# Performance work log

Hardware: AMD Instinct MI355X
Metric: run time of the kernel (lower is better)

The kernel has to match this reference:

```python
import jax, jax.numpy as jnp
import numpy as np

B, N, C = 4, 2048, 384
H = 6
D = C // H
HID = int(C * 4.0)
EPS = 1e-5


def setup_inputs() -> dict:
    key = jax.random.key(0)
    ks = jax.random.split(key, 12)
    s = lambda fan_in: 1.0 / np.sqrt(fan_in)
    return {
        "x": jax.random.normal(ks[0], (B, N, C), dtype=jnp.float32),
        "ln1_g": jnp.ones((C,), jnp.float32),
        "ln1_b": jnp.zeros((C,), jnp.float32),
        "w_qkv": jax.random.uniform(ks[1], (C, 3 * C), jnp.float32, -s(C), s(C)),
        "w_proj": jax.random.uniform(ks[2], (C, C), jnp.float32, -s(C), s(C)),
        "b_proj": jax.random.uniform(ks[3], (C,), jnp.float32, -s(C), s(C)),
        "ln2_g": jnp.ones((C,), jnp.float32),
        "ln2_b": jnp.zeros((C,), jnp.float32),
        "w_fc1": jax.random.uniform(ks[4], (C, HID), jnp.float32, -s(C), s(C)),
        "b_fc1": jax.random.uniform(ks[5], (HID,), jnp.float32, -s(C), s(C)),
        "w_fc2": jax.random.uniform(ks[6], (HID, C), jnp.float32, -s(HID), s(HID)),
        "b_fc2": jax.random.uniform(ks[7], (C,), jnp.float32, -s(HID), s(HID)),
    }


def _layernorm(x, g, b):
    mu = jnp.mean(x, axis=-1, keepdims=True)
    var = jnp.mean(jnp.square(x - mu), axis=-1, keepdims=True)
    return (x - mu) * jax.lax.rsqrt(var + EPS) * g + b


def reference(x, ln1_g, ln1_b, w_qkv, w_proj, b_proj, ln2_g, ln2_b, w_fc1, b_fc1, w_fc2, b_fc2):
    # --- attention branch (pre-norm) ---
    h = _layernorm(x, ln1_g, ln1_b)                       # [B,N,C]
    qkv = (h @ w_qkv).reshape(B, N, 3, H, D)
    q = jnp.transpose(qkv[:, :, 0], (0, 2, 1, 3))          # [B,H,N,D]
    k = jnp.transpose(qkv[:, :, 1], (0, 2, 1, 3))
    v = jnp.transpose(qkv[:, :, 2], (0, 2, 1, 3))
    scale = D ** -0.5
    attn = jnp.einsum("bhnd,bhmd->bhnm", q, k) * scale     # [B,H,N,N]
    attn = jax.nn.softmax(attn, axis=-1)
    o = jnp.einsum("bhnm,bhmd->bhnd", attn, v)             # [B,H,N,D]
    o = jnp.transpose(o, (0, 2, 1, 3)).reshape(B, N, C)
    x = x + (o @ w_proj + b_proj)
    # --- MLP branch (pre-norm) ---
    h2 = _layernorm(x, ln2_g, ln2_b)
    m = jax.nn.gelu(h2 @ w_fc1 + b_fc1, approximate=False)  # torch nn.GELU = exact erf
    x = x + (m @ w_fc2 + b_fc2)
    return x
```

## Files before the change

kernel.cpp:

```cpp
#include <hip/hip_runtime.h>

typedef __bf16 bf16x8 __attribute__((ext_vector_type(8)));
typedef float f32x4 __attribute__((ext_vector_type(4)));
typedef float f32x16 __attribute__((ext_vector_type(16)));
typedef unsigned short u16;
typedef unsigned int u32;
typedef unsigned long long u64;

#define BB 4
#define NNCTX 2048
#define CCH 384
#define NHEAD 6
#define DHEAD 64
#define HIDDIM 1536

__device__ __forceinline__ u16 f2bf(float f){
  u32 u = __builtin_bit_cast(u32, f);
  u = u + 0x7fffu + ((u >> 16) & 1u);
  return (u16)(u >> 16);
}
__device__ __forceinline__ float bf2f(u16 h){
  u32 u = ((u32)h) << 16;
  return __builtin_bit_cast(float, u);
}

union U8 { uint4 u; u16 s[8]; bf16x8 v; };
union F8 { u32 w[4]; bf16x8 v; };

__global__ __launch_bounds__(256) void cast_tr(const float* __restrict__ w0, const float* __restrict__ w1,
    const float* __restrict__ w2, const float* __restrict__ w3,
    u16* __restrict__ o0, u16* __restrict__ o1, u16* __restrict__ o2, u16* __restrict__ o3){
  __shared__ float S[64][65];
  int idx = blockIdx.x;
  const float* src; u16* dst; int K, N, kt, nt;
  if (idx < 108){ src = w0; dst = o0; K = 384; N = 1152; kt = idx / 18; nt = idx % 18; }
  else if (idx < 144){ idx -= 108; src = w1; dst = o1; K = 384; N = 384; kt = idx / 6; nt = idx % 6; }
  else if (idx < 288){ idx -= 144; src = w2; dst = o2; K = 384; N = 1536; kt = idx / 24; nt = idx % 24; }
  else { idx -= 288; src = w3; dst = o3; K = 1536; N = 384; kt = idx / 6; nt = idx % 6; }
  int t = threadIdx.x;
  int r4 = t >> 6, c = t & 63;
  int k0 = kt * 64, n0 = nt * 64;
  #pragma unroll
  for (int i = 0; i < 16; i++){
    int row = i * 4 + r4;
    S[row][c] = src[(size_t)(k0 + row) * N + n0 + c];
  }
  __syncthreads();
  #pragma unroll
  for (int i = 0; i < 16; i++){
    int row = i * 4 + r4;
    dst[(size_t)(n0 + row) * K + k0 + c] = f2bf(S[c][row]);
  }
}

__global__ __launch_bounds__(128) void ln_kernel(const float* __restrict__ x, const float* __restrict__ g,
                                                 const float* __restrict__ bb, u16* __restrict__ out){
  int row = blockIdx.x, t = threadIdx.x;
  const float* xr = x + (size_t)row * CCH;
  float v0 = xr[t], v1 = xr[t + 128], v2 = xr[t + 256];
  float s = v0 + v1 + v2;
  float q = v0 * v0 + v1 * v1 + v2 * v2;
  #pragma unroll
  for (int o = 32; o; o >>= 1){ s += __shfl_down(s, o); q += __shfl_down(q, o); }
  __shared__ float sh[4];
  if ((t & 63) == 0){ int w = t >> 6; sh[w * 2] = s; sh[w * 2 + 1] = q; }
  __syncthreads();
  float sum = sh[0] + sh[2], ssq = sh[1] + sh[3];
  float mu = sum * (1.0f / 384.0f);
  float rstd = rsqrtf(ssq * (1.0f / 384.0f) - mu * mu + 1e-5f);
  size_t base = (size_t)row * CCH;
  out[base + t]       = f2bf((v0 - mu) * rstd * g[t]       + bb[t]);
  out[base + t + 128] = f2bf((v1 - mu) * rstd * g[t + 128] + bb[t + 128]);
  out[base + t + 256] = f2bf((v2 - mu) * rstd * g[t + 256] + bb[t + 256]);
}

template<int EPI, int DBUF>
__global__ __launch_bounds__(256) void gemm_bf16(const u16* __restrict__ A, const u16* __restrict__ Bt,
    int K, int Nn, u16* __restrict__ outb, const float* __restrict__ bias,
    const float* __restrict__ resid, float* __restrict__ outf)
{
  __shared__ u16 As[DBUF + 1][64][68];
  __shared__ u16 Bs[DBUF + 1][64][68];
  int t = threadIdx.x;
  int bm = blockIdx.y * 64, bn = blockIdx.x * 64;
  int l = t & 63, w = t >> 6;
  int wm = (w >> 1) * 32, wn = (w & 1) * 32;
  f32x4 acc[2][2] = {};
  int ar0 = t >> 3, ac0 = (t & 7) * 8;
  uint4 la0, la1, lb0, lb1;
  auto LOADG = [&](int k0){
    la0 = *(const uint4*)&A[(size_t)(bm + ar0) * K + k0 + ac0];
    la1 = *(const uint4*)&A[(size_t)(bm + ar0 + 32) * K + k0 + ac0];
    lb0 = *(const uint4*)&Bt[(size_t)(bn + ar0) * K + k0 + ac0];
    lb1 = *(const uint4*)&Bt[(size_t)(bn + ar0 + 32) * K + k0 + ac0];
  };
  auto WRITEL = [&](int bf){
    *(uint4*)&As[bf][ar0][ac0]      = la0;
    *(uint4*)&As[bf][ar0 + 32][ac0] = la1;
    *(uint4*)&Bs[bf][ar0][ac0]      = lb0;
    *(uint4*)&Bs[bf][ar0 + 32][ac0] = lb1;
  };
  auto COMPUTE = [&](int bf){
    #pragma unroll
    for (int ks = 0; ks < 2; ks++){
      int kb = ks * 32 + (l >> 4) * 8;
      bf16x8 a0  = *(const bf16x8*)&As[bf][wm + (l & 15)][kb];
      bf16x8 a1  = *(const bf16x8*)&As[bf][wm + 16 + (l & 15)][kb];
      bf16x8 bb0 = *(const bf16x8*)&Bs[bf][wn + (l & 15)][kb];
      bf16x8 bb1 = *(const bf16x8*)&Bs[bf][wn + 16 + (l & 15)][kb];
      acc[0][0] = __builtin_amdgcn_mfma_f32_16x16x32_bf16(a0, bb0, acc[0][0], 0, 0, 0);
      acc[0][1] = __builtin_amdgcn_mfma_f32_16x16x32_bf16(a0, bb1, acc[0][1], 0, 0, 0);
      acc[1][0] = __builtin_amdgcn_mfma_f32_16x16x32_bf16(a1, bb0, acc[1][0], 0, 0, 0);
      acc[1][1] = __builtin_amdgcn_mfma_f32_16x16x32_bf16(a1, bb1, acc[1][1], 0, 0, 0);
    }
  };
  if constexpr (DBUF){
    int nk = K >> 6;
    LOADG(0);
    WRITEL(0);
    __syncthreads();
    for (int ki = 0; ki < nk; ki++){
      int cur = ki & 1;
      if (ki + 1 < nk) LOADG((ki + 1) << 6);
      COMPUTE(cur);
      if (ki + 1 < nk) WRITEL(cur ^ 1);
      __syncthreads();
    }
  } else {
    for (int k0 = 0; k0 < K; k0 += 64){
      __syncthreads();
      LOADG(k0);
      WRITEL(0);
      __syncthreads();
      COMPUTE(0);
    }
  }
  #pragma unroll
  for (int mi = 0; mi < 2; mi++)
  #pragma unroll
  for (int ni = 0; ni < 2; ni++)
  #pragma unroll
  for (int r = 0; r < 4; r++){
    int row = bm + wm + mi * 16 + ((l >> 4) << 2) + r;
    int col = bn + wn + ni * 16 + (l & 15);
    size_t idx = (size_t)row * Nn + col;
    float v = acc[mi][ni][r];
    if (EPI == 0){
      outb[idx] = f2bf(v);
    } else if (EPI == 1){
      outf[idx] = resid[idx] + v + bias[col];
    } else {
      v += bias[col];
      v = 0.5f * v * (1.0f + erff(v * 0.70710678118f));
      outb[idx] = f2bf(v);
    }
  }
}

#define PVSTEP(C2, O0, O1, O2, O3)                                               \
  {                                                                              \
    bf16x8 pf = *(const bf16x8*)&Ps[w][l & 31][(C2) * 16 + hi8];                 \
    u64 ta, tb, tc, td;                                                          \
    asm volatile("ds_read_b64_tr_b16 %0, %4 offset:" #O0 "\n\t"                  \
                 "ds_read_b64_tr_b16 %1, %4 offset:" #O1 "\n\t"                  \
                 "ds_read_b64_tr_b16 %2, %4 offset:" #O2 "\n\t"                  \
                 "ds_read_b64_tr_b16 %3, %4 offset:" #O3 "\n\t"                  \
                 "s_waitcnt lgkmcnt(0)"                                          \
                 : "=&v"(ta), "=&v"(tb), "=&v"(tc), "=&v"(td)                    \
                 : "v"(vtr));                                                    \
    __builtin_amdgcn_sched_barrier(0);                                           \
    F8 f0, f1;                                                                   \
    f0.w[0] = (u32)ta; f0.w[1] = (u32)(ta >> 32);                                \
    f0.w[2] = (u32)tb; f0.w[3] = (u32)(tb >> 32);                                \
    f1.w[0] = (u32)tc; f1.w[1] = (u32)(tc >> 32);                                \
    f1.w[2] = (u32)td; f1.w[3] = (u32)(td >> 32);                                \
    l_acc = __builtin_amdgcn_mfma_f32_32x32x16_bf16(pf, onesf, l_acc, 0, 0, 0);  \
    o_0 = __builtin_amdgcn_mfma_f32_32x32x16_bf16(pf, f0.v, o_0, 0, 0, 0);       \
    o_1 = __builtin_amdgcn_mfma_f32_32x32x16_bf16(pf, f1.v, o_1, 0, 0, 0);       \
  }

__global__ __launch_bounds__(256, 3) void attn_mfma(const u16* __restrict__ qkv,
    u16* __restrict__ o0buf, u16* __restrict__ o1buf, float2* __restrict__ mlbuf){
  __shared__ u16 Ks[64][68];
  __shared__ __attribute__((aligned(128))) u16 Vs[4096];
  __shared__ u16 Ps[4][32][72];
  int t = threadIdx.x;
  int w = t >> 6, l = t & 63;
  int c31 = l & 31, hi = l >> 5, hi8 = hi * 8;
  int id = blockIdx.x;
  int xcd = id & 7, slot = id >> 3;
  int qb = slot & 15;
  int group = (slot >> 4) * 8 + xcd;
  int bh = group % (BB * NHEAD);
  int sp = group / (BB * NHEAD);
  int b = bh / NHEAD, h = bh % NHEAD;
  int q0 = qb * 128;

  const float QS = 0.1803368801111716f;
  bf16x8 qf[4];
  {
    const u16* qp = qkv + (size_t)(b * NNCTX + q0 + w * 32 + c31) * 1152 + h * 64 + hi8;
    #pragma unroll
    for (int c = 0; c < 4; c++){
      U8 r; r.u = *(const uint4*)(qp + c * 16);
      #pragma unroll
      for (int j = 0; j < 8; j++) r.s[j] = f2bf(bf2f(r.s[j]) * QS);
      qf[c] = r.v;
    }
  }
  bf16x8 onesf;
  {
    U8 r;
    #pragma unroll
    for (int j = 0; j < 8; j++) r.s[j] = 0x3F80;
    onesf = r.v;
  }
  f32x16 o_0 = {}, o_1 = {};
  f32x16 l_acc = {};
  float m_r[16];
  #pragma unroll
  for (int r = 0; r < 16; r++) m_r[r] = -3.4e38f;

  const size_t kvrow = (size_t)(b * NNCTX) * 1152 + h * 64;
  int kkey = t >> 2, kdp = (t & 3) * 16;
  int vkey = t & 63, vdblk = (t >> 6) * 16;
  int vj = ((vkey & 31) << 1) | (vkey >> 5);
  int voff = (vj >> 2) * 256 + (vdblk >> 4) * 64 + (vj & 3) * 16;
  int lg = l >> 4, lr = l & 15;
  u32 vtr = (u32)(uintptr_t)(&Vs[0]) + (u32)((lg >> 1) * 1024 + (lg & 1) * 128 + lr * 8);

  uint4 kra, krb, vra, vrb;
  auto LOADT = [&](int kt){
    const u16* kp = qkv + kvrow + (size_t)(kt * 64 + kkey) * 1152 + 384 + kdp;
    kra = *(const uint4*)kp;
    krb = *(const uint4*)(kp + 8);
    const u16* vp = qkv + kvrow + (size_t)(kt * 64 + vkey) * 1152 + 768 + vdblk;
    vra = *(const uint4*)vp;
    vrb = *(const uint4*)(vp + 8);
  };
  auto WRITET = [&](){
    *(uint4*)&Ks[kkey][kdp]     = kra;
    *(uint4*)&Ks[kkey][kdp + 8] = krb;
    *(uint4*)&Vs[voff]     = vra;
    *(uint4*)&Vs[voff + 8] = vrb;
  };

  int ktbeg = sp * 16, ktend = ktbeg + 16;
  LOADT(ktbeg);
  WRITET();
  __syncthreads();

  for (int kt = ktbeg; kt < ktend; kt++){
    if (kt + 1 < ktend) LOADT(kt + 1);

    f32x16 s0 = {}, s1 = {};
    #pragma unroll
    for (int c = 0; c < 4; c++){
      bf16x8 kf0 = *(const bf16x8*)&Ks[c31][c * 16 + hi8];
      bf16x8 kf1 = *(const bf16x8*)&Ks[32 + c31][c * 16 + hi8];
      s0 = __builtin_amdgcn_mfma_f32_32x32x16_bf16(qf[c], kf0, s0, 0, 0, 0);
      s1 = __builtin_amdgcn_mfma_f32_32x32x16_bf16(qf[c], kf1, s1, 0, 0, 0);
    }
    bool ok = true;
    float rml[16];
    #pragma unroll
    for (int r = 0; r < 16; r++){
      rml[r] = fmaxf(s0[r], s1[r]);
      ok = ok && (rml[r] <= m_r[r] + 8.f);
    }
    if (!__all(ok)){
      #pragma unroll
      for (int r = 0; r < 16; r++){
        float mt = rml[r];
        mt = fmaxf(mt, __shfl_xor(mt, 1));
        mt = fmaxf(mt, __shfl_xor(mt, 2));
        mt = fmaxf(mt, __shfl_xor(mt, 4));
        mt = fmaxf(mt, __shfl_xor(mt, 8));
        mt = fmaxf(mt, __shfl_xor(mt, 16));
        float mn = fmaxf(m_r[r], mt);
        float a = __builtin_exp2f(m_r[r] - mn);
        m_r[r] = mn;
        l_acc[r] *= a;
        o_0[r] *= a;
        o_1[r] *= a;
      }
    }
    #pragma unroll
    for (int r = 0; r < 16; r++){
      float p0 = __builtin_exp2f(s0[r] - m_r[r]);
      float p1 = __builtin_exp2f(s1[r] - m_r[r]);
      int crow = (r & 3) + 8 * (r >> 2) + 4 * hi;
      *(u32*)&Ps[w][crow][c31 * 2] = (u32)f2bf(p0) | ((u32)f2bf(p1) << 16);
    }
    PVSTEP(0, 0, 512, 256, 768)
    PVSTEP(1, 2048, 2560, 2304, 2816)
    PVSTEP(2, 4096, 4608, 4352, 4864)
    PVSTEP(3, 6144, 6656, 6400, 6912)

    __syncthreads();
    if (kt + 1 < ktend) WRITET();
    __syncthreads();
  }
  u16* obuf = sp ? o1buf : o0buf;
  #pragma unroll
  for (int r = 0; r < 16; r++){
    int n = q0 + w * 32 + (r & 3) + 8 * (r >> 2) + 4 * hi;
    size_t row = (size_t)(b * NNCTX + n);
    u16* op = obuf + row * CCH + h * 64;
    op[c31]      = f2bf(o_0[r]);
    op[32 + c31] = f2bf(o_1[r]);
    if (c31 == 0)
      mlbuf[((size_t)(sp * BB * NHEAD + bh)) * NNCTX + n] = make_float2(m_r[r], l_acc[r]);
  }
}

__global__ __launch_bounds__(128) void attn_combine(const u16* __restrict__ o0, const u16* __restrict__ o1,
    const float2* __restrict__ ml, u16* __restrict__ obuf){
  __shared__ float sc0[NHEAD], sc1[NHEAD];
  int row = blockIdx.x;
  int b = row >> 11, n = row & 2047;
  int t = threadIdx.x;
  if (t < NHEAD){
    float2 a = ml[(size_t)(b * NHEAD + t) * NNCTX + n];
    float2 c = ml[(size_t)(BB * NHEAD + b * NHEAD + t) * NNCTX + n];
    float M = fmaxf(a.x, c.x);
    float e0 = exp2f(a.x - M), e1 = exp2f(c.x - M);
    float inv = 1.0f / (a.y * e0 + c.y * e1);
    sc0[t] = e0 * inv; sc1[t] = e1 * inv;
  }
  __syncthreads();
  size_t base = (size_t)row * CCH;
  #pragma unroll
  for (int i = 0; i < 3; i++){
    int c = t + i * 128;
    int h = c >> 6;
    float v = bf2f(o0[base + c]) * sc0[h] + bf2f(o1[base + c]) * sc1[h];
    obuf[base + c] = f2bf(v);
  }
}

extern "C" void kernel_launch(void* const* d_in, const int* in_sizes, int n_in,
                              void* d_out, int out_size, void* d_ws, size_t ws_size,
                              hipStream_t stream){
  const float* x      = (const float*)d_in[0];
  const float* ln1_g  = (const float*)d_in[1];
  const float* ln1_b  = (const float*)d_in[2];
  const float* w_qkv  = (const float*)d_in[3];
  const float* w_proj = (const float*)d_in[4];
  const float* b_proj = (const float*)d_in[5];
  const float* ln2_g  = (const float*)d_in[6];
  const float* ln2_b  = (const float*)d_in[7];
  const float* w_fc1  = (const float*)d_in[8];
  const float* b_fc1  = (const float*)d_in[9];
  const float* w_fc2  = (const float*)d_in[10];
  const float* b_fc2  = (const float*)d_in[11];
  float* out = (float*)d_out;

  u16* ws = (u16*)d_ws;
  u16* wqkv_bf  = ws;
  u16* wproj_bf = wqkv_bf + 442368;
  u16* wfc1_bf  = wproj_bf + 147456;
  u16* wfc2_bf  = wfc1_bf + 589824;
  u16* h_bf     = wfc2_bf + 589824;
  u16* qkv_bf   = h_bf + 3145728;
  u16* o_bf     = qkv_bf + 9437184;
  u16* opart1   = o_bf + 3145728;
  float2* mlbuf = (float2*)(opart1 + 3145728);
  u16* opart0   = h_bf;
  u16* m_bf     = qkv_bf;

  cast_tr<<<432, 256, 0, stream>>>(w_qkv, w_proj, w_fc1, w_fc2, wqkv_bf, wproj_bf, wfc1_bf, wfc2_bf);

  ln_kernel<<<8192, 128, 0, stream>>>(x, ln1_g, ln1_b, h_bf);
  gemm_bf16<0, 0><<<dim3(18, 128), 256, 0, stream>>>(h_bf, wqkv_bf, 384, 1152, qkv_bf, nullptr, nullptr, nullptr);
  attn_mfma<<<dim3(768), 256, 0, stream>>>(qkv_bf, opart0, opart1, mlbuf);
  attn_combine<<<8192, 128, 0, stream>>>(opart0, opart1, mlbuf, o_bf);
  gemm_bf16<1, 1><<<dim3(6, 128), 256, 0, stream>>>(o_bf, wproj_bf, 384, 384, nullptr, b_proj, x, out);
  ln_kernel<<<8192, 128, 0, stream>>>(out, ln2_g, ln2_b, h_bf);
  gemm_bf16<2, 0><<<dim3(24, 128), 256, 0, stream>>>(h_bf, wfc1_bf, 384, 1536, m_bf, b_fc1, nullptr, nullptr);
  gemm_bf16<1, 1><<<dim3(6, 128), 256, 0, stream>>>(m_bf, wfc2_bf, 1536, 384, nullptr, b_fc2, out, out);
}
```

Baseline: 172.2 us.

## Keep attention probabilities in registers and use 128-row GEMM tiles for QKV/FC1

The attention kernel now computes S transposed (K as the A operand), so each lane holds one query's scores. The exp'd probabilities are packed with v_cvt_pk_bf16_f32 and v_permlane32_swap directly into the MFMA A operand, removing the Ps shared-memory round trip and the per-row shuffle max reductions. The running max becomes one scalar per lane, with rescale factors broadcast by shuffle. Separately, a new gemm128 kernel with 128x64 tiles replaces the QKV and FC1 GEMMs, aiming for more reuse per block at the cost of more registers and LDS per block.

```diff
diff --git a/kernel.cpp b/kernel.cpp
--- a/kernel.cpp
+++ b/kernel.cpp
@@ -157,9 +157,97 @@
   }
 }
 
-#define PVSTEP(C2, O0, O1, O2, O3)                                               \
+template<int EPI>
+__global__ __launch_bounds__(256) void gemm128(const u16* __restrict__ A, const u16* __restrict__ Bt,
+    int K, int Nn, u16* __restrict__ outb, const float* __restrict__ bias)
+{
+  __shared__ u16 As[128][68];
+  __shared__ u16 Bs[64][68];
+  int t = threadIdx.x;
+  int bm = blockIdx.y * 128, bn = blockIdx.x * 64;
+  int l = t & 63, w = t >> 6;
+  int wm = (w >> 1) * 64, wn = (w & 1) * 32;
+  int lr = l & 15, lg4 = l >> 4;
+  f32x4 acc[4][2] = {};
+  int ar0 = t >> 3, ac0 = (t & 7) * 8;
+  uint4 la[4], lb[2];
+  auto LOADG = [&](int k0){
+    #pragma unroll
+    for (int i = 0; i < 4; i++)
+      la[i] = *(const uint4*)&A[(size_t)(bm + ar0 + i * 32) * K + k0 + ac0];
+    #pragma unroll
+    for (int i = 0; i < 2; i++)
+      lb[i] = *(const uint4*)&Bt[(size_t)(bn + ar0 + i * 32) * K + k0 + ac0];
+  };
+  auto WRITEL = [&](){
+    #pragma unroll
+    for (int i = 0; i < 4; i++) *(uint4*)&As[ar0 + i * 32][ac0] = la[i];
+    #pragma unroll
+    for (int i = 0; i < 2; i++) *(uint4*)&Bs[ar0 + i * 32][ac0] = lb[i];
+  };
+  auto COMPUTE = [&](){
+    #pragma unroll
+    for (int ks = 0; ks < 2; ks++){
+      int kb = ks * 32 + lg4 * 8;
+      bf16x8 bb0 = *(const bf16x8*)&Bs[wn + lr][kb];
+      bf16x8 bb1 = *(const bf16x8*)&Bs[wn + 16 + lr][kb];
+      #pragma unroll
+      for (int mi = 0; mi < 4; mi++){
+        bf16x8 am = *(const bf16x8*)&As[wm + mi * 16 + lr][kb];
+        acc[mi][0] = __builtin_amdgcn_mfma_f32_16x16x32_bf16(am, bb0, acc[mi][0], 0, 0, 0);
+        acc[mi][1] = __builtin_amdgcn_mfma_f32_16x16x32_bf16(am, bb1, acc[mi][1], 0, 0, 0);
+      }
+    }
+  };
+  int nk = K >> 6;
+  LOADG(0);
+  WRITEL();
+  __syncthreads();
+  for (int ki = 0; ki < nk; ki++){
+    if (ki + 1 < nk) LOADG((ki + 1) << 6);
+    COMPUTE();
+    __syncthreads();
+    if (ki + 1 < nk) WRITEL();
+    __syncthreads();
+  }
+  #pragma unroll
+  for (int mi = 0; mi < 4; mi++)
+  #pragma unroll
+  for (int ni = 0; ni < 2; ni++)
+  #pragma unroll
+  for (int r = 0; r < 4; r++){
+    int row = bm + wm + mi * 16 + (l >> 4) * 4 + r;
+    int col = bn + wn + ni * 16 + lr;
+    size_t idx = (size_t)row * Nn + col;
+    float v = acc[mi][ni][r];
+    if (EPI == 0){
+      outb[idx] = f2bf(v);
+    } else {
+      v += bias[col];
+      v = 0.5f * v * (1.0f + erff(v * 0.70710678118f));
+      outb[idx] = f2bf(v);
+    }
+  }
+}
+
+#define PVSTEP(O0, O1, O2, O3, SX, BASE)                                         \
   {                                                                              \
-    bf16x8 pf = *(const bf16x8*)&Ps[w][l & 31][(C2) * 16 + hi8];                 \
+    float p0 = __builtin_exp2f(SX[BASE + 0] - m_q);                              \
+    float p1 = __builtin_exp2f(SX[BASE + 1] - m_q);                              \
+    float p2 = __builtin_exp2f(SX[BASE + 2] - m_q);                              \
+    float p3 = __builtin_exp2f(SX[BASE + 3] - m_q);                              \
+    float p4 = __builtin_exp2f(SX[BASE + 4] - m_q);                              \
+    float p5 = __builtin_exp2f(SX[BASE + 5] - m_q);                              \
+    float p6 = __builtin_exp2f(SX[BASE + 6] - m_q);                              \
+    float p7 = __builtin_exp2f(SX[BASE + 7] - m_q);                              \
+    u32 wa0, wa1, wb0, wb1;                                                      \
+    asm("v_cvt_pk_bf16_f32 %0, %1, %2" : "=v"(wa0) : "v"(p0), "v"(p1));          \
+    asm("v_cvt_pk_bf16_f32 %0, %1, %2" : "=v"(wa1) : "v"(p2), "v"(p3));          \
+    asm("v_cvt_pk_bf16_f32 %0, %1, %2" : "=v"(wb0) : "v"(p4), "v"(p5));          \
+    asm("v_cvt_pk_bf16_f32 %0, %1, %2" : "=v"(wb1) : "v"(p6), "v"(p7));          \
+    asm("v_permlane32_swap_b32 %0, %1" : "+v"(wa0), "+v"(wb0));                  \
+    asm("v_permlane32_swap_b32 %0, %1" : "+v"(wa1), "+v"(wb1));                  \
+    F8 pa; pa.w[0] = wa0; pa.w[1] = wa1; pa.w[2] = wb0; pa.w[3] = wb1;           \
     u64 ta, tb, tc, td;                                                          \
     asm volatile("ds_read_b64_tr_b16 %0, %4 offset:" #O0 "\n\t"                  \
                  "ds_read_b64_tr_b16 %1, %4 offset:" #O1 "\n\t"                  \
@@ -174,16 +262,15 @@
     f0.w[2] = (u32)tb; f0.w[3] = (u32)(tb >> 32);                                \
     f1.w[0] = (u32)tc; f1.w[1] = (u32)(tc >> 32);                                \
     f1.w[2] = (u32)td; f1.w[3] = (u32)(td >> 32);                                \
-    l_acc = __builtin_amdgcn_mfma_f32_32x32x16_bf16(pf, onesf, l_acc, 0, 0, 0);  \
-    o_0 = __builtin_amdgcn_mfma_f32_32x32x16_bf16(pf, f0.v, o_0, 0, 0, 0);       \
-    o_1 = __builtin_amdgcn_mfma_f32_32x32x16_bf16(pf, f1.v, o_1, 0, 0, 0);       \
+    l_acc = __builtin_amdgcn_mfma_f32_32x32x16_bf16(pa.v, onesf, l_acc, 0, 0, 0);\
+    o_0 = __builtin_amdgcn_mfma_f32_32x32x16_bf16(pa.v, f0.v, o_0, 0, 0, 0);     \
+    o_1 = __builtin_amdgcn_mfma_f32_32x32x16_bf16(pa.v, f1.v, o_1, 0, 0, 0);     \
   }
 
 __global__ __launch_bounds__(256, 3) void attn_mfma(const u16* __restrict__ qkv,
     u16* __restrict__ o0buf, u16* __restrict__ o1buf, float2* __restrict__ mlbuf){
   __shared__ u16 Ks[64][68];
   __shared__ __attribute__((aligned(128))) u16 Vs[4096];
-  __shared__ u16 Ps[4][32][72];
   int t = threadIdx.x;
   int w = t >> 6, l = t & 63;
   int c31 = l & 31, hi = l >> 5, hi8 = hi * 8;
@@ -217,17 +304,14 @@
   }
   f32x16 o_0 = {}, o_1 = {};
   f32x16 l_acc = {};
-  float m_r[16];
-  #pragma unroll
-  for (int r = 0; r < 16; r++) m_r[r] = -3.4e38f;
+  float m_q = -3.4e38f;
 
   const size_t kvrow = (size_t)(b * NNCTX) * 1152 + h * 64;
   int kkey = t >> 2, kdp = (t & 3) * 16;
-  int vkey = t & 63, vdblk = (t >> 6) * 16;
-  int vj = ((vkey & 31) << 1) | (vkey >> 5);
-  int voff = (vj >> 2) * 256 + (vdblk >> 4) * 64 + (vj & 3) * 16;
-  int lg = l >> 4, lr = l & 15;
-  u32 vtr = (u32)(uintptr_t)(&Vs[0]) + (u32)((lg >> 1) * 1024 + (lg & 1) * 128 + lr * 8);
+  int vkey = t & 63, vdblk = w * 16;
+  int voff = (vkey >> 2) * 256 + w * 64 + (vkey & 3) * 16;
+  int lg = l >> 4, lr16 = l & 15;
+  u32 vtr = (u32)(uintptr_t)(&Vs[0]) + (u32)((lg >> 1) * 1024 + (lg & 1) * 128 + lr16 * 8);
 
   uint4 kra, krb, vra, vrb;
   auto LOADT = [&](int kt){
@@ -258,44 +342,30 @@
     for (int c = 0; c < 4; c++){
       bf16x8 kf0 = *(const bf16x8*)&Ks[c31][c * 16 + hi8];
       bf16x8 kf1 = *(const bf16x8*)&Ks[32 + c31][c * 16 + hi8];
-      s0 = __builtin_amdgcn_mfma_f32_32x32x16_bf16(qf[c], kf0, s0, 0, 0, 0);
-      s1 = __builtin_amdgcn_mfma_f32_32x32x16_bf16(qf[c], kf1, s1, 0, 0, 0);
-    }
-    bool ok = true;
-    float rml[16];
-    #pragma unroll
-    for (int r = 0; r < 16; r++){
-      rml[r] = fmaxf(s0[r], s1[r]);
-      ok = ok && (rml[r] <= m_r[r] + 8.f);
-    }
-    if (!__all(ok)){
+      s0 = __builtin_amdgcn_mfma_f32_32x32x16_bf16(kf0, qf[c], s0, 0, 0, 0);
+      s1 = __builtin_amdgcn_mfma_f32_32x32x16_bf16(kf1, qf[c], s1, 0, 0, 0);
+    }
+    float px = fmaxf(s0[0], s0[1]);
+    #pragma unroll
+    for (int r = 2; r < 16; r++) px = fmaxf(px, s0[r]);
+    #pragma unroll
+    for (int r = 0; r < 16; r++) px = fmaxf(px, s1[r]);
+    px = fmaxf(px, __shfl_xor(px, 32));
+    if (!__all(px <= m_q + 8.f)){
+      float mn = fmaxf(m_q, px);
+      float a = __builtin_exp2f(m_q - mn);
+      m_q = mn;
       #pragma unroll
       for (int r = 0; r < 16; r++){
-        float mt = rml[r];
-        mt = fmaxf(mt, __shfl_xor(mt, 1));
-        mt = fmaxf(mt, __shfl_xor(mt, 2));
-        mt = fmaxf(mt, __shfl_xor(mt, 4));
-        mt = fmaxf(mt, __shfl_xor(mt, 8));
-        mt = fmaxf(mt, __shfl_xor(mt, 16));
-        float mn = fmaxf(m_r[r], mt);
-        float a = __builtin_exp2f(m_r[r] - mn);
-        m_r[r] = mn;
-        l_acc[r] *= a;
-        o_0[r] *= a;
-        o_1[r] *= a;
+        int cr = (r & 3) + 8 * (r >> 2) + 4 * hi;
+        float ar = __shfl(a, cr);
+        o_0[r] *= ar; o_1[r] *= ar; l_acc[r] *= ar;
       }
     }
-    #pragma unroll
-    for (int r = 0; r < 16; r++){
-      float p0 = __builtin_exp2f(s0[r] - m_r[r]);
-      float p1 = __builtin_exp2f(s1[r] - m_r[r]);
-      int crow = (r & 3) + 8 * (r >> 2) + 4 * hi;
-      *(u32*)&Ps[w][crow][c31 * 2] = (u32)f2bf(p0) | ((u32)f2bf(p1) << 16);
-    }
-    PVSTEP(0, 0, 512, 256, 768)
-    PVSTEP(1, 2048, 2560, 2304, 2816)
-    PVSTEP(2, 4096, 4608, 4352, 4864)
-    PVSTEP(3, 6144, 6656, 6400, 6912)
+    PVSTEP(0, 512, 256, 768, s0, 0)
+    PVSTEP(2048, 2560, 2304, 2816, s0, 8)
+    PVSTEP(4096, 4608, 4352, 4864, s1, 0)
+    PVSTEP(6144, 6656, 6400, 6912, s1, 8)
 
     __syncthreads();
     if (kt + 1 < ktend) WRITET();
@@ -304,13 +374,15 @@
   u16* obuf = sp ? o1buf : o0buf;
   #pragma unroll
   for (int r = 0; r < 16; r++){
-    int n = q0 + w * 32 + (r & 3) + 8 * (r >> 2) + 4 * hi;
+    int cr = (r & 3) + 8 * (r >> 2) + 4 * hi;
+    float mr = __shfl(m_q, cr);
+    int n = q0 + w * 32 + cr;
     size_t row = (size_t)(b * NNCTX + n);
     u16* op = obuf + row * CCH + h * 64;
     op[c31]      = f2bf(o_0[r]);
     op[32 + c31] = f2bf(o_1[r]);
     if (c31 == 0)
-      mlbuf[((size_t)(sp * BB * NHEAD + bh)) * NNCTX + n] = make_float2(m_r[r], l_acc[r]);
+      mlbuf[((size_t)(sp * BB * NHEAD + bh)) * NNCTX + n] = make_float2(mr, l_acc[r]);
   }
 }
 
@@ -372,11 +444,11 @@
   cast_tr<<<432, 256, 0, stream>>>(w_qkv, w_proj, w_fc1, w_fc2, wqkv_bf, wproj_bf, wfc1_bf, wfc2_bf);
 
   ln_kernel<<<8192, 128, 0, stream>>>(x, ln1_g, ln1_b, h_bf);
-  gemm_bf16<0, 0><<<dim3(18, 128), 256, 0, stream>>>(h_bf, wqkv_bf, 384, 1152, qkv_bf, nullptr, nullptr, nullptr);
+  gemm128<0><<<dim3(18, 64), 256, 0, stream>>>(h_bf, wqkv_bf, 384, 1152, qkv_bf, nullptr);
   attn_mfma<<<dim3(768), 256, 0, stream>>>(qkv_bf, opart0, opart1, mlbuf);
   attn_combine<<<8192, 128, 0, stream>>>(opart0, opart1, mlbuf, o_bf);
   gemm_bf16<1, 1><<<dim3(6, 128), 256, 0, stream>>>(o_bf, wproj_bf, 384, 384, nullptr, b_proj, x, out);
   ln_kernel<<<8192, 128, 0, stream>>>(out, ln2_g, ln2_b, h_bf);
-  gemm_bf16<2, 0><<<dim3(24, 128), 256, 0, stream>>>(h_bf, wfc1_bf, 384, 1536, m_bf, b_fc1, nullptr, nullptr);
+  gemm128<2><<<dim3(24, 64), 256, 0, stream>>>(h_bf, wfc1_bf, 384, 1536, m_bf, b_fc1);
   gemm_bf16<1, 1><<<dim3(6, 128), 256, 0, stream>>>(m_bf, wfc2_bf, 1536, 384, nullptr, b_fc2, out, out);
 }
```

Result: slower. 226.2 us (+31.4%).
